# Optimization experiments

Measured on AMD Instinct MI355X. Metric: run time of the kernel, lower is better.

Reference implementation:

```python
import jax, jax.numpy as jnp
import numpy as np

B, L, HID = 2, 2048, 4096
NH, NKV, HD = 16, 4, 64
BLOCK = 16
THETA = 8000000.0
EPS = 1e-6
NEG = jnp.finfo(jnp.float32).min


def _rope_tables(theta, L, hd):
    inv_freq = 1.0 / (theta ** (np.arange(0, hd, 2, dtype=np.float32) / hd))  # [hd/2]
    t = np.arange(L, dtype=np.float32)
    freqs = np.outer(t, inv_freq)                      # [L, hd/2]
    emb = np.concatenate([freqs, freqs], axis=-1)      # [L, hd]
    return jnp.asarray(np.cos(emb)), jnp.asarray(np.sin(emb))


def setup_inputs() -> dict:
    key = jax.random.key(0)
    k1, k2, k3 = jax.random.split(key, 3)
    hidden_states = jax.random.normal(k1, (B, L, HID), dtype=jnp.float32)
    Wqkv = jax.random.normal(k2, (HID, (NH + 2 * NKV) * HD), dtype=jnp.float32) * 0.006
    Wo = jax.random.normal(k3, (NH * HD, HID), dtype=jnp.float32) * 0.006
    q_norm_w = jnp.ones((HD,), dtype=jnp.float32)
    k_norm_w = jnp.ones((HD,), dtype=jnp.float32)
    # block-diagonal causal additive mask [1,1,L,L]
    idx = jnp.arange(L)
    same_block = (idx[:, None] // BLOCK) == (idx[None, :] // BLOCK)
    causal = idx[:, None] >= idx[None, :]
    attention_mask = jnp.where(same_block & causal, 0.0, NEG)[None, None].astype(jnp.float32)
    cos1, sin1 = _rope_tables(THETA, L, HD)
    cos = jnp.broadcast_to(cos1[None], (B, L, HD))
    sin = jnp.broadcast_to(sin1[None], (B, L, HD))
    return {"hidden_states": hidden_states, "attention_mask": attention_mask,
            "cos": cos, "sin": sin, "Wqkv": Wqkv, "Wo": Wo,
            "q_norm_w": q_norm_w, "k_norm_w": k_norm_w}


def _rms_norm(x, w):
    xf = x.astype(jnp.float32)
    var = jnp.mean(xf * xf, axis=-1, keepdims=True)
    return (xf * jax.lax.rsqrt(var + EPS)).astype(x.dtype) * w


def _rotate_half(x):
    x1, x2 = jnp.split(x, 2, axis=-1)
    return jnp.concatenate([-x2, x1], axis=-1)


def reference(hidden_states, attention_mask, cos, sin, Wqkv, Wo, q_norm_w, k_norm_w):
    Bc, Lc, _ = hidden_states.shape
    qkv = hidden_states @ Wqkv                                # [B,L,(NH+2NKV)*HD]
    qkv = qkv.reshape(Bc, Lc, NH + 2 * NKV, HD)
    q, k, v = jnp.split(qkv, [NH, NH + NKV], axis=2)
    q = q.transpose(0, 2, 1, 3)                               # [B,NH,L,HD]
    k = k.transpose(0, 2, 1, 3)                               # [B,NKV,L,HD]
    v = v.transpose(0, 2, 1, 3)
    q = _rms_norm(q, q_norm_w)
    k = _rms_norm(k, k_norm_w)
    c = cos[:, None]                                          # [B,1,L,HD]
    s = sin[:, None]
    q = q * c + _rotate_half(q) * s
    k = k * c + _rotate_half(k) * s
    groups = NH // NKV
    k = jnp.repeat(k, groups, axis=1)                         # [B,NH,L,HD]
    v = jnp.repeat(v, groups, axis=1)
    scale = 1.0 / jnp.sqrt(jnp.float32(HD))
    scores = jnp.einsum('bhqd,bhkd->bhqk', q, k) * scale + attention_mask
    probs = jax.nn.softmax(scores, axis=-1)
    out = jnp.einsum('bhqk,bhkd->bhqd', probs, v)             # [B,NH,L,HD]
    out = out.transpose(0, 2, 1, 3).reshape(Bc, Lc, NH * HD)
    return out @ Wo
```

## Files before the change

kernel.cpp:

```cpp
#include <hip/hip_runtime.h>
#include <hip/hip_bf16.h>
#include <cstdint>

#define B_SZ   2
#define L_SEQ  2048
#define HID    4096
#define NH     16
#define NKV    4
#define HD     64
#define NQKV   (NH + 2*NKV)
#define QKV_N  (NQKV*HD)
#define O_N    (NH*HD)
#define M_ROWS (B_SZ*L_SEQ)
#define EPSV   1e-6f

typedef __bf16  bf16x8_t  __attribute__((ext_vector_type(8)));
typedef float   f32x4_t   __attribute__((ext_vector_type(4)));
typedef unsigned short ushort8_t __attribute__((ext_vector_type(8)));

__device__ __forceinline__ unsigned short f2b(float f) {
    union { float f; uint32_t u; } v; v.f = f;
    uint32_t r = v.u + 0x7FFFu + ((v.u >> 16) & 1u);
    return (unsigned short)(r >> 16);
}
__device__ __forceinline__ float b2f(unsigned short u) {
    union { uint32_t u; float f; } v; v.u = ((uint32_t)u) << 16;
    return v.f;
}

__device__ __forceinline__ void gload_lds16(const void* g, void* l) {
    __builtin_amdgcn_global_load_lds(
        (__attribute__((address_space(1))) void*)(g),
        (__attribute__((address_space(3))) void*)(l),
        16, 0, 0);
}

#define BARF() do { asm volatile("" ::: "memory"); \
                    __builtin_amdgcn_s_barrier();  \
                    asm volatile("" ::: "memory"); } while (0)

template <int N> __device__ __forceinline__ void vmcnt_wait() {
    if constexpr (N == 4)       asm volatile("s_waitcnt vmcnt(4)"  ::: "memory");
    else if constexpr (N == 5)  asm volatile("s_waitcnt vmcnt(5)"  ::: "memory");
    else if constexpr (N == 6)  asm volatile("s_waitcnt vmcnt(6)"  ::: "memory");
    else if constexpr (N == 8)  asm volatile("s_waitcnt vmcnt(8)"  ::: "memory");
    else if constexpr (N == 10) asm volatile("s_waitcnt vmcnt(10)" ::: "memory");
    else if constexpr (N == 12) asm volatile("s_waitcnt vmcnt(12)" ::: "memory");
    else                        asm volatile("s_waitcnt vmcnt(0)"  ::: "memory");
}

__global__ __launch_bounds__(256) void cvt_f32_bf16(const float* __restrict__ in,
                                                    unsigned short* __restrict__ out,
                                                    int n8) {
    int i = blockIdx.x * 256 + threadIdx.x;
    if (i >= n8) return;
    const float4* p = (const float4*)(in + (size_t)i * 8);
    float4 a = p[0], b = p[1];
    ushort8_t o;
    o[0]=f2b(a.x); o[1]=f2b(a.y); o[2]=f2b(a.z); o[3]=f2b(a.w);
    o[4]=f2b(b.x); o[5]=f2b(b.y); o[6]=f2b(b.z); o[7]=f2b(b.w);
    *(ushort8_t*)(out + (size_t)i * 8) = o;
}

__global__ __launch_bounds__(256) void transpose_f32_bf16(const float* __restrict__ in,
                                                          unsigned short* __restrict__ out,
                                                          int R, int C) {
    __shared__ float t[32][33];
    const int c0 = blockIdx.x * 32;
    const int r0 = blockIdx.y * 32;
    const int tx = threadIdx.x & 31;
    const int ty = threadIdx.x >> 5;
    #pragma unroll
    for (int i = 0; i < 32; i += 8)
        t[ty + i][tx] = in[(size_t)(r0 + ty + i) * C + c0 + tx];
    __syncthreads();
    #pragma unroll
    for (int i = 0; i < 32; i += 8)
        out[(size_t)(c0 + ty + i) * R + r0 + tx] = f2b(t[tx][ty + i]);
}

template <int BM, int BN, int BK, int NBUF, int NWM, int NWN, bool OBF16, typename OutT>
__global__ __launch_bounds__(512, 2)
void gemm_sb(const unsigned short* __restrict__ A,
             const unsigned short* __restrict__ Bt,
             OutT* __restrict__ C, int M, int N, int K) {
    constexpr int WM    = BM / NWM;
    constexpr int WN    = BN / NWN;
    constexpr int AF    = WM / 16;
    constexpr int BF    = WN / 16;
    constexpr int KK    = BK / 32;
    constexpr int BUF   = (BM + BN) * BK;
    constexpr int ROWS  = 4096 / BK;
    constexpr int AR    = BM / ROWS;
    constexpr int BR    = BN / ROWS;
    constexpr int RNDS  = AR + BR;
    constexpr int DEPTH = NBUF - 2;

    __shared__ unsigned short smem[NBUF * BUF];

    const int tid  = threadIdx.x;
    const int lane = tid & 63;
    const int wave = tid >> 6;
    const int wm   = wave / NWN;
    const int wn   = wave % NWN;
    const int fr   = lane & 15;
    const int fq   = lane >> 4;

    const int nbx = N / BN;
    int bid = blockIdx.x;
    const int cpx = gridDim.x >> 3;
    bid = (bid & 7) * cpx + (bid >> 3);
    const int bx = bid % nbx, by = bid / nbx;
    const int m0 = by * BM, n0 = bx * BN;

    const int srow = tid / (BK / 8);
    const int sch  = tid & (BK / 8 - 1);
    const int ssw  = (BK == 64) ? (srow & 7) : ((srow >> 1) & 3);
    const int scs  = (sch ^ ssw) << 3;
    const unsigned short* gA = A  + (size_t)(m0 + srow) * K + scs;
    const unsigned short* gB = Bt + (size_t)(n0 + srow) * K + scs;

    const int frsw = (BK == 64) ? (fr & 7) : ((fr >> 1) & 3);

    f32x4_t acc[AF][BF];
    #pragma unroll
    for (int m = 0; m < AF; m++)
        #pragma unroll
        for (int n = 0; n < BF; n++)
            acc[m][n] = (f32x4_t){0.f, 0.f, 0.f, 0.f};

    const int NT = K / BK;

    auto STAGE = [&](int T) {
        const int pb = (T % NBUF) * BUF;
        #pragma unroll
        for (int q = 0; q < AR; ++q)
            gload_lds16(gA + (size_t)(q * ROWS) * K + (size_t)T * BK,
                        &smem[pb + q * 4096 + tid * 8]);
        #pragma unroll
        for (int q = 0; q < BR; ++q)
            gload_lds16(gB + (size_t)(q * ROWS) * K + (size_t)T * BK,
                        &smem[pb + BM * BK + q * 4096 + tid * 8]);
    };

    #pragma unroll
    for (int pt = 0; pt < NBUF - 1; ++pt) STAGE(pt);
    vmcnt_wait<DEPTH * RNDS>();

    for (int t = 0; t < NT; ++t) {
        const int sb = (t % NBUF) * BUF;
        BARF();

        bf16x8_t aF[KK][AF], bF[KK][BF];
        #pragma unroll
        for (int kk = 0; kk < KK; ++kk) {
            const int cxk = (((kk * 4 + fq) ^ frsw)) << 3;
            #pragma unroll
            for (int mm = 0; mm < AF; ++mm)
                aF[kk][mm] = *(const bf16x8_t*)&smem[sb + (wm*WM + mm*16 + fr)*BK + cxk];
            #pragma unroll
            for (int nn = 0; nn < BF; ++nn)
                bF[kk][nn] = *(const bf16x8_t*)&smem[sb + BM*BK + (wn*WN + nn*16 + fr)*BK + cxk];
        }

        if (t + NBUF - 1 < NT) STAGE(t + NBUF - 1);

        #pragma unroll
        for (int kk = 0; kk < KK; ++kk) {
            __builtin_amdgcn_s_setprio(1);
            #pragma unroll
            for (int mm = 0; mm < AF; ++mm)
                #pragma unroll
                for (int nn = 0; nn < BF; ++nn)
                    acc[mm][nn] = __builtin_amdgcn_mfma_f32_16x16x32_bf16(
                        aF[kk][mm], bF[kk][nn], acc[mm][nn], 0, 0, 0);
            __builtin_amdgcn_s_setprio(0);
        }

        if constexpr (DEPTH == 2) {
            if (t + 3 < NT)      { vmcnt_wait<2 * RNDS>(); }
            else if (t + 2 < NT) { vmcnt_wait<RNDS>(); }
            else if (t + 1 < NT) { vmcnt_wait<0>(); }
        } else {
            if (t + 2 < NT)      { vmcnt_wait<RNDS>(); }
            else if (t + 1 < NT) { vmcnt_wait<0>(); }
        }
    }

    const int crow = m0 + wm * WM + fq * 4;
    const int ccol = n0 + wn * WN + fr;
    #pragma unroll
    for (int m = 0; m < AF; m++)
        #pragma unroll
        for (int n = 0; n < BF; n++)
            #pragma unroll
            for (int rr = 0; rr < 4; rr++) {
                const size_t idx = (size_t)(crow + m*16 + rr) * N + ccol + n*16;
                if constexpr (OBF16) C[idx] = (OutT)f2b(acc[m][n][rr]);
                else                 C[idx] = (OutT)acc[m][n][rr];
            }
}

__global__ __launch_bounds__(64) void attn_fused(const unsigned short* __restrict__ qkv,
                                                 const float* __restrict__ cosb,
                                                 const float* __restrict__ sinb,
                                                 const float* __restrict__ qw,
                                                 const float* __restrict__ kw,
                                                 unsigned short* __restrict__ out) {
    const int h    = blockIdx.x & (NH - 1);
    const int blk  = (blockIdx.x >> 4) & 127;
    const int b    = blockIdx.x >> 11;
    const int pos0 = blk * 16;
    const int kvh  = h >> 2;

    const int lane = threadIdx.x;
    const int r    = lane >> 2;
    const int qp   = lane & 3;
    const int d0   = qp * 16;

    __shared__ float qs[16][65];
    __shared__ float ks[16][65];
    __shared__ float vs[16][65];
    __shared__ float ps[16][17];

    const size_t rowb = ((size_t)(b * L_SEQ + pos0 + r)) * NQKV;
    const unsigned short* qptr = qkv + (rowb + h) * HD + d0;
    const unsigned short* kptr = qkv + (rowb + NH + kvh) * HD + d0;
    const unsigned short* vptr = qkv + (rowb + NH + NKV + kvh) * HD + d0;
    const size_t csrow = ((size_t)(b * L_SEQ + pos0 + r)) * HD + d0;

    float q[16], k[16], v[16], cs[16], sn[16];
    {
        ushort8_t q0 = *(const ushort8_t*)&qptr[0], q1 = *(const ushort8_t*)&qptr[8];
        ushort8_t k0 = *(const ushort8_t*)&kptr[0], k1 = *(const ushort8_t*)&kptr[8];
        ushort8_t v0 = *(const ushort8_t*)&vptr[0], v1 = *(const ushort8_t*)&vptr[8];
        #pragma unroll
        for (int i = 0; i < 8; i++) {
            q[i] = b2f(q0[i]); q[i+8] = b2f(q1[i]);
            k[i] = b2f(k0[i]); k[i+8] = b2f(k1[i]);
            v[i] = b2f(v0[i]); v[i+8] = b2f(v1[i]);
        }
        #pragma unroll
        for (int i = 0; i < 16; i += 4) {
            *(float4*)&cs[i] = *(const float4*)&cosb[csrow + i];
            *(float4*)&sn[i] = *(const float4*)&sinb[csrow + i];
        }
    }

    float sq = 0.f, sk = 0.f;
    #pragma unroll
    for (int i = 0; i < 16; i++) { sq += q[i]*q[i]; sk += k[i]*k[i]; }
    sq += __shfl_xor(sq, 1); sq += __shfl_xor(sq, 2);
    sk += __shfl_xor(sk, 1); sk += __shfl_xor(sk, 2);
    const float rq = rsqrtf(sq * (1.f / HD) + EPSV);
    const float rk = rsqrtf(sk * (1.f / HD) + EPSV);

    const float sgn = (qp < 2) ? -1.f : 1.f;
    #pragma unroll
    for (int i = 0; i < 16; i++) {
        float qn = q[i] * rq * qw[d0 + i];
        float kn = k[i] * rk * kw[d0 + i];
        float qo = __shfl_xor(qn, 2);
        float ko = __shfl_xor(kn, 2);
        qs[r][d0 + i] = qn * cs[i] + sgn * qo * sn[i];
        ks[r][d0 + i] = kn * cs[i] + sgn * ko * sn[i];
        vs[r][d0 + i] = v[i];
    }
    __syncthreads();

    float sc[4] = {0.f, 0.f, 0.f, 0.f};
    for (int d = 0; d < 64; d++) {
        const float qd = qs[r][d];
        sc[0] += qd * ks[qp     ][d];
        sc[1] += qd * ks[qp +  4][d];
        sc[2] += qd * ks[qp +  8][d];
        sc[3] += qd * ks[qp + 12][d];
    }
    #pragma unroll
    for (int cc = 0; cc < 4; cc++) {
        const int c = qp + cc * 4;
        sc[cc] = (c <= r) ? sc[cc] * 0.125f : -3.0e38f;
    }
    float mx = fmaxf(fmaxf(sc[0], sc[1]), fmaxf(sc[2], sc[3]));
    mx = fmaxf(mx, __shfl_xor(mx, 1));
    mx = fmaxf(mx, __shfl_xor(mx, 2));
    float e[4], sum = 0.f;
    #pragma unroll
    for (int cc = 0; cc < 4; cc++) { e[cc] = __expf(sc[cc] - mx); sum += e[cc]; }
    sum += __shfl_xor(sum, 1); sum += __shfl_xor(sum, 2);
    const float inv = 1.f / sum;
    #pragma unroll
    for (int cc = 0; cc < 4; cc++) ps[r][qp + cc * 4] = e[cc] * inv;
    __syncthreads();

    float o[16];
    #pragma unroll
    for (int i = 0; i < 16; i++) o[i] = 0.f;
    #pragma unroll
    for (int c = 0; c < 16; c++) {
        const float p = ps[r][c];
        #pragma unroll
        for (int i = 0; i < 16; i++) o[i] += p * vs[c][d0 + i];
    }

    __attribute__((aligned(16))) unsigned short ob[16];
    #pragma unroll
    for (int i = 0; i < 16; i++) ob[i] = f2b(o[i]);
    unsigned short* optr = out + (((size_t)(b * L_SEQ + pos0 + r) * NH + h) * HD) + d0;
    *(uint4*)optr       = *(uint4*)&ob[0];
    *((uint4*)optr + 1) = *(uint4*)&ob[8];
}

extern "C" void kernel_launch(void* const* d_in, const int* in_sizes, int n_in,
                              void* d_out, int out_size, void* d_ws, size_t ws_size,
                              hipStream_t stream) {
    const float* hid  = (const float*)d_in[0];
    const float* cosb = (const float*)d_in[2];
    const float* sinb = (const float*)d_in[3];
    const float* Wqkv = (const float*)d_in[4];
    const float* Wo   = (const float*)d_in[5];
    const float* qw   = (const float*)d_in[6];
    const float* kw   = (const float*)d_in[7];
    float* outp = (float*)d_out;

    char* ws = (char*)d_ws;
    unsigned short* Hb    = (unsigned short*)ws; ws += (size_t)M_ROWS * HID * 2;
    unsigned short* WqkvT = (unsigned short*)ws; ws += (size_t)QKV_N * HID * 2;
    unsigned short* WoT   = (unsigned short*)ws; ws += (size_t)HID * O_N * 2;
    unsigned short* qkvb  = (unsigned short*)ws; ws += (size_t)M_ROWS * QKV_N * 2;
    unsigned short* attnb = (unsigned short*)ws;

    {
        int n8 = (M_ROWS * HID) / 8;
        cvt_f32_bf16<<<(n8 + 255) / 256, 256, 0, stream>>>(hid, Hb, n8);
    }
    transpose_f32_bf16<<<dim3(QKV_N / 32, HID / 32), 256, 0, stream>>>(Wqkv, WqkvT, HID, QKV_N);
    transpose_f32_bf16<<<dim3(HID / 32, O_N / 32),  256, 0, stream>>>(Wo,   WoT,   O_N, HID);

    gemm_sb<256, 128, 64, 3, 4, 2, true, unsigned short>
        <<<dim3((M_ROWS / 256) * (QKV_N / 128)), 512, 0, stream>>>
        (Hb, WqkvT, qkvb, M_ROWS, QKV_N, HID);

    attn_fused<<<dim3(B_SZ * (L_SEQ / 16) * NH), 64, 0, stream>>>(qkvb, cosb, sinb, qw, kw, attnb);

    gemm_sb<256, 256, 32, 4, 2, 4, false, float>
        <<<dim3((M_ROWS / 256) * (HID / 256)), 512, 0, stream>>>
        (attnb, WoT, outp, M_ROWS, HID, O_N);
}
```

Before: 152.4 us.

## Interleave per-k LDS fragment loads with MFMA and retune GEMM tile shapes

Adds a template flag that selects between loading every k-slice fragment up front (burst) and loading fragments one k-slice at a time, interleaved with the MFMA work. The non-burst mode is meant to cut register pressure and overlap LDS reads with matrix math. The QKV GEMM moves to 128x192 tiles with interleaved loads, which launches more blocks for the narrow N=1536 output. The output-projection GEMM moves to 256x128x64 tiles with 3 buffers using burst loads. The risk is lower reuse per tile and different occupancy.

```diff
diff --git a/kernel.cpp b/kernel.cpp
--- a/kernel.cpp
+++ b/kernel.cpp
@@ -79,7 +79,8 @@
         out[(size_t)(c0 + ty + i) * R + r0 + tx] = f2b(t[tx][ty + i]);
 }
 
-template <int BM, int BN, int BK, int NBUF, int NWM, int NWN, bool OBF16, typename OutT>
+template <int BM, int BN, int BK, int NBUF, int NWM, int NWN, bool BURST,
+          bool OBF16, typename OutT>
 __global__ __launch_bounds__(512, 2)
 void gemm_sb(const unsigned short* __restrict__ A,
              const unsigned short* __restrict__ Bt,
@@ -151,30 +152,53 @@
         const int sb = (t % NBUF) * BUF;
         BARF();
 
-        bf16x8_t aF[KK][AF], bF[KK][BF];
-        #pragma unroll
-        for (int kk = 0; kk < KK; ++kk) {
-            const int cxk = (((kk * 4 + fq) ^ frsw)) << 3;
+        if constexpr (BURST) {
+            bf16x8_t aF[KK][AF], bF[KK][BF];
             #pragma unroll
-            for (int mm = 0; mm < AF; ++mm)
-                aF[kk][mm] = *(const bf16x8_t*)&smem[sb + (wm*WM + mm*16 + fr)*BK + cxk];
+            for (int kk = 0; kk < KK; ++kk) {
+                const int cxk = (((kk * 4 + fq) ^ frsw)) << 3;
+                #pragma unroll
+                for (int mm = 0; mm < AF; ++mm)
+                    aF[kk][mm] = *(const bf16x8_t*)&smem[sb + (wm*WM + mm*16 + fr)*BK + cxk];
+                #pragma unroll
+                for (int nn = 0; nn < BF; ++nn)
+                    bF[kk][nn] = *(const bf16x8_t*)&smem[sb + BM*BK + (wn*WN + nn*16 + fr)*BK + cxk];
+            }
+            if (t + NBUF - 1 < NT) STAGE(t + NBUF - 1);
             #pragma unroll
-            for (int nn = 0; nn < BF; ++nn)
-                bF[kk][nn] = *(const bf16x8_t*)&smem[sb + BM*BK + (wn*WN + nn*16 + fr)*BK + cxk];
-        }
-
-        if (t + NBUF - 1 < NT) STAGE(t + NBUF - 1);
-
-        #pragma unroll
-        for (int kk = 0; kk < KK; ++kk) {
-            __builtin_amdgcn_s_setprio(1);
+            for (int kk = 0; kk < KK; ++kk) {
+                __builtin_amdgcn_s_setprio(1);
+                #pragma unroll
+                for (int mm = 0; mm < AF; ++mm)
+                    #pragma unroll
+                    for (int nn = 0; nn < BF; ++nn)
+                        acc[mm][nn] = __builtin_amdgcn_mfma_f32_16x16x32_bf16(
+                            aF[kk][mm], bF[kk][nn], acc[mm][nn], 0, 0, 0);
+                __builtin_amdgcn_s_setprio(0);
+            }
+        } else {
             #pragma unroll
-            for (int mm = 0; mm < AF; ++mm)
+            for (int kk = 0; kk < KK; ++kk) {
+                const int cxk = (((kk * 4 + fq) ^ frsw)) << 3;
+                bf16x8_t aF[AF], bF[BF];
+                #pragma unroll
+                for (int mm = 0; mm < AF; ++mm)
+                    aF[mm] = *(const bf16x8_t*)&smem[sb + (wm*WM + mm*16 + fr)*BK + cxk];
                 #pragma unroll
                 for (int nn = 0; nn < BF; ++nn)
-                    acc[mm][nn] = __builtin_amdgcn_mfma_f32_16x16x32_bf16(
-                        aF[kk][mm], bF[kk][nn], acc[mm][nn], 0, 0, 0);
-            __builtin_amdgcn_s_setprio(0);
+                    bF[nn] = *(const bf16x8_t*)&smem[sb + BM*BK + (wn*WN + nn*16 + fr)*BK + cxk];
+
+                if (kk == 0 && t + NBUF - 1 < NT) STAGE(t + NBUF - 1);
+
+                __builtin_amdgcn_s_setprio(1);
+                #pragma unroll
+                for (int mm = 0; mm < AF; ++mm)
+                    #pragma unroll
+                    for (int nn = 0; nn < BF; ++nn)
+                        acc[mm][nn] = __builtin_amdgcn_mfma_f32_16x16x32_bf16(
+                            aF[mm], bF[nn], acc[mm][nn], 0, 0, 0);
+                __builtin_amdgcn_s_setprio(0);
+            }
         }
 
         if constexpr (DEPTH == 2) {
@@ -337,13 +361,13 @@
     transpose_f32_bf16<<<dim3(QKV_N / 32, HID / 32), 256, 0, stream>>>(Wqkv, WqkvT, HID, QKV_N);
     transpose_f32_bf16<<<dim3(HID / 32, O_N / 32),  256, 0, stream>>>(Wo,   WoT,   O_N, HID);
 
-    gemm_sb<256, 128, 64, 3, 4, 2, true, unsigned short>
-        <<<dim3((M_ROWS / 256) * (QKV_N / 128)), 512, 0, stream>>>
+    gemm_sb<128, 192, 64, 3, 2, 4, false, true, unsigned short>
+        <<<dim3((M_ROWS / 128) * (QKV_N / 192)), 512, 0, stream>>>
         (Hb, WqkvT, qkvb, M_ROWS, QKV_N, HID);
 
     attn_fused<<<dim3(B_SZ * (L_SEQ / 16) * NH), 64, 0, stream>>>(qkvb, cosb, sinb, qw, kw, attnb);
 
-    gemm_sb<256, 256, 32, 4, 2, 4, false, float>
-        <<<dim3((M_ROWS / 256) * (HID / 256)), 512, 0, stream>>>
+    gemm_sb<256, 128, 64, 3, 4, 2, true, false, float>
+        <<<dim3((M_ROWS / 256) * (HID / 128)), 512, 0, stream>>>
         (attnb, WoT, outp, M_ROWS, HID, O_N);
 }
```

Result: no change. 151.9 us (-0.3%).
